# Kernel optimization log

Measured on AMD Instinct MI355X. Metric: run time of the kernel, lower is better.

## Reference

```python
import jax, jax.numpy as jnp
import numpy as np

COST_CLASS, COST_BBOX, COST_MASK = 1.0, 5.0, 2.0
EPS = 1e-6


def setup_inputs() -> dict:
    key = jax.random.key(0)
    k = jax.random.split(key, 8)
    B, Q, M, C1, H, W = 8, 300, 100, 81, 128, 128
    pred_logits = jax.random.normal(k[0], (B, Q, C1), jnp.float32)
    # boxes as valid xyxy in [0,1]: lo in [0,.5], size in [0,.5]
    plo = jax.random.uniform(k[1], (B, Q, 2)) * 0.5
    psz = jax.random.uniform(k[2], (B, Q, 2)) * 0.5
    pred_boxes = jnp.concatenate([plo, plo + psz], axis=-1)
    pred_masks = jax.random.normal(k[3], (B, Q, H, W), jnp.float32)
    gt_labels = jax.random.randint(k[4], (B, M), 0, C1, dtype=jnp.int32)
    glo = jax.random.uniform(k[5], (B, M, 2)) * 0.5
    gsz = jax.random.uniform(k[6], (B, M, 2)) * 0.5
    gt_boxes = jnp.concatenate([glo, glo + gsz], axis=-1)
    gt_masks = (jax.random.uniform(k[7], (B, M, H, W)) > 0.5).astype(jnp.float32)
    valid = jnp.ones((B, M), jnp.bool_)
    return dict(pred_logits=pred_logits, pred_boxes=pred_boxes, pred_masks=pred_masks,
                gt_labels=gt_labels, gt_boxes=gt_boxes, gt_masks=gt_masks, valid=valid)


def _giou(b1, b2):
    # b1 [Q,4], b2 [M,4] (xyxy) -> [Q,M] generalized IoU
    lt = jnp.maximum(b1[:, None, :2], b2[None, :, :2])
    rb = jnp.minimum(b1[:, None, 2:], b2[None, :, 2:])
    wh = jnp.clip(rb - lt, 0.0)
    inter = wh[..., 0] * wh[..., 1]
    a1 = (b1[:, 2] - b1[:, 0]) * (b1[:, 3] - b1[:, 1])
    a2 = (b2[:, 2] - b2[:, 0]) * (b2[:, 3] - b2[:, 1])
    union = a1[:, None] + a2[None, :] - inter
    iou = inter / (union + EPS)
    ltm = jnp.minimum(b1[:, None, :2], b2[None, :, :2])
    rbm = jnp.maximum(b1[:, None, 2:], b2[None, :, 2:])
    whm = jnp.clip(rbm - ltm, 0.0)
    am = whm[..., 0] * whm[..., 1]
    return iou - (am - union) / (am + EPS)


@jax.jit
def _cost_matrix(pred_logits, pred_boxes, pred_masks, gt_labels, gt_boxes, gt_masks):
    B, Q = pred_logits.shape[:2]
    M = gt_labels.shape[1]
    probs = jax.nn.softmax(pred_logits, axis=-1)                      # [B,Q,C+1]
    idx = jnp.broadcast_to(gt_labels[:, None, :].astype(jnp.int32), (B, Q, M))
    cost_class = -jnp.take_along_axis(probs, idx, axis=2)             # [B,Q,M]
    # L1 cdist
    cost_bbox = jnp.abs(pred_boxes[:, :, None, :] - gt_boxes[:, None, :, :]).sum(-1)
    cost_giou = -jax.vmap(_giou)(pred_boxes, gt_boxes)                # [B,Q,M]
    # dice cost
    pm = jax.nn.sigmoid(pred_masks).reshape(B, Q, -1)                 # [B,Q,HW]
    gm = gt_masks.reshape(B, M, -1).astype(pm.dtype)                  # [B,M,HW]
    num = 2.0 * jnp.einsum('bqc,bmc->bqm', pm, gm)
    den = pm.sum(-1)[:, :, None] + gm.sum(-1)[:, None, :]
    cost_mask = 1.0 - num / (den + EPS)
    # NOTE: faithful to source quirk -- giou term is folded into cost_bbox
    # and therefore weighted by COST_BBOX.
    return (COST_CLASS * cost_class + COST_BBOX * (cost_bbox + cost_giou)
            + COST_MASK * cost_mask)


def _hungarian(cost):
    # Jonker-Volgenant style shortest-augmenting-path assignment (e-maxx).
    # cost: np [n,m] with n <= m. Returns p[m]: row assigned to each col (-1 if none).
    n, m = cost.shape
    u = np.zeros(n)
    v = np.zeros(m)
    p = np.full(m, -1, np.int64)
    for i in range(n):
        minv = np.full(m, np.inf)
        way = np.full(m, -1, np.int64)
        used = np.zeros(m, bool)
        cur_row, j0 = i, -1
        while True:
            cur = cost[cur_row] - u[cur_row] - v
            upd = (~used) & (cur < minv)
            minv[upd] = cur[upd]
            way[upd] = j0
            mv = np.where(used, np.inf, minv)
            j1 = int(np.argmin(mv))
            delta = mv[j1]
            u[i] += delta
            uj = np.nonzero(used)[0]
            if uj.size:
                u[p[uj]] += delta
                v[uj] -= delta
            minv[~used] -= delta
            used[j1] = True
            j0 = j1
            cur_row = p[j1]
            if cur_row == -1:
                break
        j = j0
        while j != -1:
            jp = way[j]
            p[j] = p[jp] if jp != -1 else i
            j = jp
    return p


def reference(pred_logits, pred_boxes, pred_masks, gt_labels, gt_boxes, gt_masks, valid):
    # valid is all-ones (num_gt == max_objects for every sample), so the
    # per-sample variable-size slicing in the torch loop reduces to full M.
    C = _cost_matrix(pred_logits, pred_boxes, pred_masks, gt_labels, gt_boxes, gt_masks)
    Cn = np.asarray(C, dtype=np.float64)
    preds, gts = [], []
    for b in range(Cn.shape[0]):
        # solve on transpose: rows = gt (M=100) <= cols = queries (Q=300)
        p = _hungarian(Cn[b].T)            # p[q] = matched gt index or -1
        q = np.nonzero(p >= 0)[0]          # sorted pred indices (scipy convention)
        preds.append(q)
        gts.append(p[q])
    pred_idx = jnp.asarray(np.stack(preds), dtype=jnp.int32)  # [B, M]
    gt_idx = jnp.asarray(np.stack(gts), dtype=jnp.int32)      # [B, M]
    return C, pred_idx, gt_idx
```

## Files before the change

kernel.cpp:

```cpp
#include <hip/hip_runtime.h>

#define HW 16384
#define NQ 300
#define NM 100
#define NB 8
#define NC 81
#define KCH 1024
#define NKC 16
#define CTP 304

typedef __attribute__((ext_vector_type(8))) short frag8;
typedef __attribute__((ext_vector_type(4))) float float4v;
typedef __attribute__((ext_vector_type(4))) unsigned short ushort4v;

__device__ __forceinline__ unsigned short f2bf(float f) {
  union { float f; unsigned u; } c; c.f = f;
  unsigned r = c.u + 0x7FFFu + ((c.u >> 16) & 1u);
  return (unsigned short)(r >> 16);
}

__global__ __launch_bounds__(256) void prep_kernel(
    const float* __restrict__ pmask, const float* __restrict__ gmask,
    unsigned short* __restrict__ pm, unsigned short* __restrict__ gm,
    float* __restrict__ psum, float* __restrict__ gsum) {
  int row = blockIdx.x;
  int t = threadIdx.x;
  bool isP = row < NB * NQ;
  const float* srcf = isP ? (pmask + (size_t)row * HW)
                          : (gmask + (size_t)(row - NB * NQ) * HW);
  unsigned short* dst = isP ? (pm + (size_t)row * HW)
                            : (gm + (size_t)(row - NB * NQ) * HW);
  const float4v* src = (const float4v*)srcf;
  float s = 0.f;
  for (int i = t; i < HW / 4; i += 256) {
    float4v x = src[i];
    float y0, y1, y2, y3;
    if (isP) {
      y0 = 1.f / (1.f + __expf(-x.x));
      y1 = 1.f / (1.f + __expf(-x.y));
      y2 = 1.f / (1.f + __expf(-x.z));
      y3 = 1.f / (1.f + __expf(-x.w));
    } else { y0 = x.x; y1 = x.y; y2 = x.z; y3 = x.w; }
    s += (y0 + y1) + (y2 + y3);
    ushort4v o = { f2bf(y0), f2bf(y1), f2bf(y2), f2bf(y3) };
    *(ushort4v*)(dst + i * 4) = o;
  }
  for (int off = 32; off > 0; off >>= 1) s += __shfl_xor(s, off, 64);
  __shared__ float red[4];
  int wave = t >> 6, lane = t & 63;
  if (lane == 0) red[wave] = s;
  __syncthreads();
  if (t == 0) {
    float tot = (red[0] + red[1]) + (red[2] + red[3]);
    if (isP) psum[row] = tot; else gsum[row - NB * NQ] = tot;
  }
}

__global__ __launch_bounds__(256) void softmax_kernel(
    const float* __restrict__ logits, float* __restrict__ probs) {
  int wave = threadIdx.x >> 6, lane = threadIdx.x & 63;
  int row = blockIdx.x * 4 + wave;
  const float* in = logits + (size_t)row * NC;
  float x0 = (lane < NC) ? in[lane] : -1e30f;
  float x1 = (lane + 64 < NC) ? in[lane + 64] : -1e30f;
  float mx = fmaxf(x0, x1);
  for (int off = 32; off > 0; off >>= 1) mx = fmaxf(mx, __shfl_xor(mx, off, 64));
  float e0 = (lane < NC) ? __expf(x0 - mx) : 0.f;
  float e1 = (lane + 64 < NC) ? __expf(x1 - mx) : 0.f;
  float s = e0 + e1;
  for (int off = 32; off > 0; off >>= 1) s += __shfl_xor(s, off, 64);
  float inv = 1.f / s;
  if (lane < NC) probs[(size_t)row * NC + lane] = e0 * inv;
  if (lane + 64 < NC) probs[(size_t)row * NC + lane + 64] = e1 * inv;
}

__global__ __launch_bounds__(64) void dot_kernel(
    const unsigned short* __restrict__ pm, const unsigned short* __restrict__ gm,
    float* __restrict__ dotv) {
  int qt = blockIdx.x;
  int b = blockIdx.y >> 4, kc = blockIdx.y & 15;
  int lane = threadIdx.x;
  int q0 = qt * 16;
  int row_a = q0 + (lane & 15);
  int ra = (row_a < NQ) ? row_a : NQ - 1;
  int koff = (lane >> 4) * 8;
  const unsigned short* pA = pm + ((size_t)b * NQ + ra) * HW + kc * KCH + koff;
  const unsigned short* pB0 = gm + (size_t)b * NM * HW + kc * KCH + koff;
  const unsigned short* pB[7];
#pragma unroll
  for (int mt = 0; mt < 7; ++mt) {
    int row_b = mt * 16 + (lane & 15);
    int rb = (row_b < NM) ? row_b : NM - 1;
    pB[mt] = pB0 + (size_t)rb * HW;
  }
  float4v acc[7];
#pragma unroll
  for (int mt = 0; mt < 7; ++mt) acc[mt] = (float4v){0.f, 0.f, 0.f, 0.f};
#pragma unroll 2
  for (int k = 0; k < KCH; k += 32) {
    frag8 a = *(const frag8*)(pA + k);
#pragma unroll
    for (int mt = 0; mt < 7; ++mt) {
      frag8 bb = *(const frag8*)(pB[mt] + k);
      acc[mt] = __builtin_amdgcn_mfma_f32_16x16x32_bf16(a, bb, acc[mt], 0, 0, 0);
    }
  }
#pragma unroll
  for (int mt = 0; mt < 7; ++mt) {
    int cm = mt * 16 + (lane & 15);
    if (cm < NM) {
#pragma unroll
      for (int r = 0; r < 4; ++r) {
        int cq = q0 + (lane >> 4) * 4 + r;
        if (cq < NQ)
          unsafeAtomicAdd(&dotv[((size_t)b * NQ + cq) * NM + cm], acc[mt][r]);
      }
    }
  }
}

__global__ __launch_bounds__(256) void combine_kernel(
    const float* __restrict__ dotv, const float* __restrict__ psum,
    const float* __restrict__ gsum, const float* __restrict__ probs,
    const int* __restrict__ labels, const float* __restrict__ pboxes,
    const float* __restrict__ gboxes, float* __restrict__ outC,
    float* __restrict__ ct) {
  int idx = blockIdx.x * 256 + threadIdx.x;
  if (idx >= NB * NQ * NM) return;
  int b = idx / (NQ * NM);
  int r = idx - b * (NQ * NM);
  int q = r / NM;
  int m = r - q * NM;
  float num = 2.f * dotv[idx];
  float den = psum[b * NQ + q] + gsum[b * NM + m];
  float cmask = 1.f - num / (den + 1e-6f);
  int lab = labels[b * NM + m];
  float cclass = -probs[((size_t)b * NQ + q) * NC + lab];
  const float* pb = pboxes + ((size_t)b * NQ + q) * 4;
  const float* gb = gboxes + ((size_t)b * NM + m) * 4;
  float p0 = pb[0], p1 = pb[1], p2 = pb[2], p3 = pb[3];
  float g0 = gb[0], g1 = gb[1], g2 = gb[2], g3 = gb[3];
  float cbbox = fabsf(p0 - g0) + fabsf(p1 - g1) + fabsf(p2 - g2) + fabsf(p3 - g3);
  float iw = fmaxf(fminf(p2, g2) - fmaxf(p0, g0), 0.f);
  float ih = fmaxf(fminf(p3, g3) - fmaxf(p1, g1), 0.f);
  float inter = iw * ih;
  float a1 = (p2 - p0) * (p3 - p1), a2 = (g2 - g0) * (g3 - g1);
  float uni = a1 + a2 - inter;
  float iou = inter / (uni + 1e-6f);
  float aw = fmaxf(fmaxf(p2, g2) - fminf(p0, g0), 0.f);
  float ah = fmaxf(fmaxf(p3, g3) - fminf(p1, g1), 0.f);
  float am = aw * ah;
  float giou = iou - (am - uni) / (am + 1e-6f);
  float C = cclass + 5.f * (cbbox - giou) + 2.f * cmask;
  outC[idx] = C;
  ct[((size_t)b * NM + m) * CTP + q] = C;
}

extern __shared__ char hsmem[];
__global__ __launch_bounds__(64) void hungarian_kernel(
    const float* __restrict__ ct, float* __restrict__ out) {
  float* cost = (float*)hsmem;
  float* u = (float*)(hsmem + 121600);
  int* p = (int*)(hsmem + 122000);
  int* way = (int*)(hsmem + 123280);
  int* colA = (int*)(hsmem + 124560);
  int* rowUsed = (int*)(hsmem + 124960);
  int* colUsed = (int*)(hsmem + 125360);
  const int b = blockIdx.x;
  const int lane = threadIdx.x;
  const float* a = ct + (size_t)b * NM * CTP;

  for (int i = lane; i < NM * CTP; i += 64) cost[i] = a[i];
  for (int k = lane; k < NM; k += 64) rowUsed[k] = 0;
  float v[5], minv[5];
  int usedR[5];
#pragma unroll
  for (int w = 0; w < 5; ++w) {
    p[lane + 64 * w] = -1;
    colUsed[lane + 64 * w] = 0;
    v[w] = 0.f;
  }
  __syncthreads();

  for (int i = lane; i < NM; i += 64) {
    float mv = __builtin_inff();
    int cj = 0;
    for (int j = 0; j < NQ; ++j) {
      float c = cost[i * CTP + j];
      if (c < mv) { mv = c; cj = j; }
    }
    u[i] = mv;
    colA[i] = cj;
  }
  __syncthreads();
  if (lane == 0) {
    for (int i = 0; i < NM; ++i) {
      int j = colA[i];
      if (!colUsed[j]) { colUsed[j] = 1; p[j] = i; rowUsed[i] = 1; }
    }
  }
  __syncthreads();

  for (int i = 0; i < NM; ++i) {
    if (rowUsed[i]) continue;
#pragma unroll
    for (int w = 0; w < 5; ++w) {
      int j = lane + 64 * w;
      minv[w] = __builtin_inff();
      usedR[w] = (j >= NQ) ? 1 : 0;
      way[j] = -1;
    }
    int cur_row = i;
    int j0 = -1;
    __builtin_amdgcn_wave_barrier();
    while (true) {
      float urow = u[cur_row];
      unsigned long long best = ~0ull;
#pragma unroll
      for (int w = 0; w < 5; ++w) {
        if (!usedR[w]) {
          int j = lane + 64 * w;
          float cur = cost[cur_row * CTP + j] - urow - v[w];
          if (cur < minv[w]) { minv[w] = cur; way[j] = j0; }
          unsigned sb = __float_as_uint(minv[w]);
          sb = (sb >> 31) ? ~sb : (sb | 0x80000000u);
          unsigned long long key = ((unsigned long long)sb << 32) | (unsigned)j;
          if (key < best) best = key;
        }
      }
      for (int off = 32; off > 0; off >>= 1) {
        unsigned long long o = __shfl_xor(best, off, 64);
        if (o < best) best = o;
      }
      int j1 = (int)(best & 0xFFFFFFFFu);
      unsigned sb = (unsigned)(best >> 32);
      float delta = __uint_as_float((sb >> 31) ? (sb ^ 0x80000000u) : ~sb);
      __builtin_amdgcn_wave_barrier();
#pragma unroll
      for (int w = 0; w < 5; ++w) {
        int j = lane + 64 * w;
        if (j < NQ) {
          if (usedR[w]) {
            v[w] -= delta;
            int pj = p[j];
            u[pj] += delta;
          } else {
            minv[w] -= delta;
          }
        }
      }
      if (lane == 0) u[i] += delta;
      __builtin_amdgcn_wave_barrier();
#pragma unroll
      for (int w = 0; w < 5; ++w) {
        if (lane + 64 * w == j1) usedR[w] = 1;
      }
      int nr = p[j1];
      j0 = j1;
      if (nr < 0) break;
      cur_row = nr;
    }
    __builtin_amdgcn_wave_barrier();
    if (lane == 0) {
      int j = j0;
      while (j != -1) {
        int jp = way[j];
        p[j] = (jp != -1) ? p[jp] : i;
        j = jp;
      }
    }
    __syncthreads();
  }
  if (lane == 0) {
    float* po = out + NB * NQ * NM + b * NM;
    float* go = out + NB * NQ * NM + NB * NM + b * NM;
    int cnt = 0;
    for (int j = 0; j < NQ; ++j) {
      int pj = p[j];
      if (pj >= 0) { po[cnt] = (float)j; go[cnt] = (float)pj; ++cnt; }
    }
  }
}

extern "C" void kernel_launch(void* const* d_in, const int* in_sizes, int n_in,
                              void* d_out, int out_size, void* d_ws, size_t ws_size,
                              hipStream_t stream) {
  const float* logits = (const float*)d_in[0];
  const float* pboxes = (const float*)d_in[1];
  const float* pmask  = (const float*)d_in[2];
  const int*   labels = (const int*)d_in[3];
  const float* gboxes = (const float*)d_in[4];
  const float* gmask  = (const float*)d_in[5];
  float* out = (float*)d_out;
  char* ws = (char*)d_ws;

  unsigned short* pm   = (unsigned short*)(ws + 0);
  unsigned short* gmb  = (unsigned short*)(ws + 78643200);
  float* psum  = (float*)(ws + 104857600);
  float* gsum  = (float*)(ws + 104867200);
  float* probs = (float*)(ws + 104870400);
  float* dotv  = (float*)(ws + 105648000);
  float* ct    = (float*)(ws + 106608000);

  hipFuncSetAttribute(reinterpret_cast<const void*>(hungarian_kernel),
                      hipFuncAttributeMaxDynamicSharedMemorySize, 126640);

  hipMemsetAsync(dotv, 0, NB * NQ * NM * sizeof(float), stream);
  hipLaunchKernelGGL(prep_kernel, dim3(NB * NQ + NB * NM), dim3(256), 0, stream,
                     pmask, gmask, pm, gmb, psum, gsum);
  hipLaunchKernelGGL(softmax_kernel, dim3(600), dim3(256), 0, stream, logits, probs);
  hipLaunchKernelGGL(dot_kernel, dim3(19, NB * NKC), dim3(64), 0, stream, pm, gmb, dotv);
  hipLaunchKernelGGL(combine_kernel, dim3((NB * NQ * NM + 255) / 256), dim3(256), 0, stream,
                     dotv, psum, gsum, probs, labels, pboxes, gboxes, out, ct);
  hipLaunchKernelGGL(hungarian_kernel, dim3(NB), dim3(64), 126640, stream, ct, out);
}
```

Before: 519.6 us.

## Add auction-style augmenting-row reduction and lazy dual updates to Hungarian solver

Replaces the serial greedy column initialization with a parallel atomicMin-based assignment. It then adds a JVC-style augmenting row reduction pass that uses first/second minimum reductions over a queue of free rows, capped at 192 pops. The shortest-path phase now keeps cumulative distances and applies dual updates once at the end of each augmentation instead of on every step. The final index compaction is parallelized with ballots. The aim is to cut the serial single-wave Hungarian time, which likely dominates, at the cost of more complex logic. Tie-breaking may differ from the reference when there are equal-cost assignments.

```diff
diff --git a/kernel.cpp b/kernel.cpp
--- a/kernel.cpp
+++ b/kernel.cpp
@@ -159,70 +159,151 @@
 extern __shared__ char hsmem[];
 __global__ __launch_bounds__(64) void hungarian_kernel(
     const float* __restrict__ ct, float* __restrict__ out) {
-  float* cost = (float*)hsmem;
-  float* u = (float*)(hsmem + 121600);
-  int* p = (int*)(hsmem + 122000);
-  int* way = (int*)(hsmem + 123280);
-  int* colA = (int*)(hsmem + 124560);
-  int* rowUsed = (int*)(hsmem + 124960);
-  int* colUsed = (int*)(hsmem + 125360);
+  float* cost   = (float*)hsmem;
+  float* u      = (float*)(hsmem + 121600);
+  int*   p      = (int*)(hsmem + 122000);
+  int*   way    = (int*)(hsmem + 123280);
+  int*   colOwn = (int*)(hsmem + 124560);
+  int*   rowUsed= (int*)(hsmem + 125840);
+  int*   queue  = (int*)(hsmem + 126240);
+  int*   qmisc  = (int*)(hsmem + 127840);
   const int b = blockIdx.x;
   const int lane = threadIdx.x;
-  const float* a = ct + (size_t)b * NM * CTP;
-
-  for (int i = lane; i < NM * CTP; i += 64) cost[i] = a[i];
-  for (int k = lane; k < NM; k += 64) rowUsed[k] = 0;
-  float v[5], minv[5];
-  int usedR[5];
+  const float INF = __builtin_inff();
+
+  {
+    const float4v* a4 = (const float4v*)(ct + (size_t)b * NM * CTP);
+    float4v* c4 = (float4v*)cost;
+    for (int i = lane; i < NM * CTP / 4; i += 64) c4[i] = a4[i];
+  }
 #pragma unroll
   for (int w = 0; w < 5; ++w) {
     p[lane + 64 * w] = -1;
-    colUsed[lane + 64 * w] = 0;
-    v[w] = 0.f;
-  }
+    colOwn[lane + 64 * w] = 0x7fffffff;
+  }
+  if (lane == 0) { qmisc[0] = 0; qmisc[1] = 0; }
+  float v[5];
+#pragma unroll
+  for (int w = 0; w < 5; ++w) v[w] = 0.f;
   __syncthreads();
 
-  for (int i = lane; i < NM; i += 64) {
-    float mv = __builtin_inff();
-    int cj = 0;
+  int rarg0 = 0, rarg1 = 0;
+  {
+    int i = lane;
+    float mv = INF; int cj = 0;
     for (int j = 0; j < NQ; ++j) {
       float c = cost[i * CTP + j];
       if (c < mv) { mv = c; cj = j; }
     }
-    u[i] = mv;
-    colA[i] = cj;
-  }
+    u[i] = mv; rarg0 = cj;
+  }
+  if (lane < NM - 64) {
+    int i = lane + 64;
+    float mv = INF; int cj = 0;
+    for (int j = 0; j < NQ; ++j) {
+      float c = cost[i * CTP + j];
+      if (c < mv) { mv = c; cj = j; }
+    }
+    u[i] = mv; rarg1 = cj;
+  }
+  atomicMin(&colOwn[rarg0], lane);
+  if (lane < NM - 64) atomicMin(&colOwn[rarg1], lane + 64);
   __syncthreads();
-  if (lane == 0) {
-    for (int i = 0; i < NM; ++i) {
-      int j = colA[i];
-      if (!colUsed[j]) { colUsed[j] = 1; p[j] = i; rowUsed[i] = 1; }
+  int free0 = 0, free1 = 0;
+  {
+    bool won = (colOwn[rarg0] == lane);
+    if (won) p[rarg0] = lane;
+    rowUsed[lane] = won ? 1 : 0;
+    free0 = won ? 0 : 1;
+  }
+  if (lane < NM - 64) {
+    bool won = (colOwn[rarg1] == lane + 64);
+    if (won) p[rarg1] = lane + 64;
+    rowUsed[lane + 64] = won ? 1 : 0;
+    free1 = won ? 0 : 1;
+  }
+  {
+    unsigned long long m0 = __ballot(free0 != 0);
+    if (free0) queue[__popcll(m0 & ((1ull << lane) - 1ull))] = lane;
+    int base = (int)__popcll(m0);
+    unsigned long long m1 = __ballot(free1 != 0);
+    if (free1) queue[base + (int)__popcll(m1 & ((1ull << lane) - 1ull))] = lane + 64;
+    base += (int)__popcll(m1);
+    if (lane == 0) qmisc[1] = base;
+  }
+
+  int pops = 0;
+  while (true) {
+    __syncthreads();
+    int h = qmisc[0], t = qmisc[1];
+    if (h >= t || pops >= 192) break;
+    int i = queue[h];
+    ++pops;
+    if (lane == 0) qmisc[0] = h + 1;
+    float m1 = INF, m2 = INF; int jl = 0;
+#pragma unroll
+    for (int w = 0; w < 5; ++w) {
+      int j = lane + 64 * w;
+      float tt = (j < NQ) ? (cost[i * CTP + j] - v[w]) : INF;
+      if (tt < m1) { m2 = m1; m1 = tt; jl = j; } else if (tt < m2) m2 = tt;
+    }
+    unsigned long long best;
+    {
+      unsigned sb = __float_as_uint(m1);
+      sb = (sb >> 31) ? ~sb : (sb | 0x80000000u);
+      best = ((unsigned long long)sb << 32) | (unsigned)jl;
+    }
+    for (int off = 32; off > 0; off >>= 1) {
+      unsigned long long o = __shfl_xor(best, off, 64);
+      if (o < best) best = o;
+    }
+    int j1 = (int)(best & 0xFFFFFFFFu);
+    float m1g;
+    {
+      unsigned sb = (unsigned)(best >> 32);
+      m1g = __uint_as_float((sb >> 31) ? (sb ^ 0x80000000u) : ~sb);
+    }
+    float c2 = (jl == j1) ? m2 : m1;
+    for (int off = 32; off > 0; off >>= 1) c2 = fminf(c2, __shfl_xor(c2, off, 64));
+    float delta = (c2 > m1g) ? (c2 - m1g) : 0.f;
+    int i1 = p[j1];
+    if (i1 >= 0 && delta <= 0.f) {
+      if (lane == 0) u[i] = c2;
+      continue;
+    }
+#pragma unroll
+    for (int w = 0; w < 5; ++w) if (lane + 64 * w == j1) v[w] -= delta;
+    if (lane == 0) {
+      u[i] = c2;
+      p[j1] = i;
+      rowUsed[i] = 1;
+      if (i1 >= 0) { rowUsed[i1] = 0; queue[t] = i1; qmisc[1] = t + 1; }
     }
   }
   __syncthreads();
 
   for (int i = 0; i < NM; ++i) {
     if (rowUsed[i]) continue;
+    float dv[5]; int usedR[5];
 #pragma unroll
     for (int w = 0; w < 5; ++w) {
       int j = lane + 64 * w;
-      minv[w] = __builtin_inff();
+      dv[w] = INF;
       usedR[w] = (j >= NQ) ? 1 : 0;
       way[j] = -1;
     }
-    int cur_row = i;
-    int j0 = -1;
-    __builtin_amdgcn_wave_barrier();
+    float S = 0.f;
+    int nr = i, j0 = -1;
     while (true) {
-      float urow = u[cur_row];
+      float urow = u[nr];
       unsigned long long best = ~0ull;
 #pragma unroll
       for (int w = 0; w < 5; ++w) {
         if (!usedR[w]) {
           int j = lane + 64 * w;
-          float cur = cost[cur_row * CTP + j] - urow - v[w];
-          if (cur < minv[w]) { minv[w] = cur; way[j] = j0; }
-          unsigned sb = __float_as_uint(minv[w]);
+          float cand = S + cost[nr * CTP + j] - urow - v[w];
+          if (cand < dv[w]) { dv[w] = cand; way[j] = j0; }
+          unsigned sb = __float_as_uint(dv[w]);
           sb = (sb >> 31) ? ~sb : (sb | 0x80000000u);
           unsigned long long key = ((unsigned long long)sb << 32) | (unsigned)j;
           if (key < best) best = key;
@@ -233,34 +314,29 @@
         if (o < best) best = o;
       }
       int j1 = (int)(best & 0xFFFFFFFFu);
-      unsigned sb = (unsigned)(best >> 32);
-      float delta = __uint_as_float((sb >> 31) ? (sb ^ 0x80000000u) : ~sb);
-      __builtin_amdgcn_wave_barrier();
-#pragma unroll
-      for (int w = 0; w < 5; ++w) {
-        int j = lane + 64 * w;
-        if (j < NQ) {
-          if (usedR[w]) {
-            v[w] -= delta;
-            int pj = p[j];
-            u[pj] += delta;
-          } else {
-            minv[w] -= delta;
-          }
-        }
-      }
-      if (lane == 0) u[i] += delta;
-      __builtin_amdgcn_wave_barrier();
-#pragma unroll
-      for (int w = 0; w < 5; ++w) {
-        if (lane + 64 * w == j1) usedR[w] = 1;
-      }
-      int nr = p[j1];
+      {
+        unsigned sb = (unsigned)(best >> 32);
+        S = __uint_as_float((sb >> 31) ? (sb ^ 0x80000000u) : ~sb);
+      }
+#pragma unroll
+      for (int w = 0; w < 5; ++w) if (lane + 64 * w == j1) usedR[w] = 1;
       j0 = j1;
-      if (nr < 0) break;
-      cur_row = nr;
-    }
-    __builtin_amdgcn_wave_barrier();
+      int nr2 = p[j1];
+      if (nr2 < 0) break;
+      nr = nr2;
+    }
+#pragma unroll
+    for (int w = 0; w < 5; ++w) {
+      int j = lane + 64 * w;
+      if (j < NQ && usedR[w]) {
+        float amt = S - dv[w];
+        v[w] -= amt;
+        int pj = p[j];
+        if (pj >= 0) u[pj] += amt;
+      }
+    }
+    if (lane == 0) u[i] += S;
+    __syncthreads();
     if (lane == 0) {
       int j = j0;
       while (j != -1) {
@@ -268,16 +344,26 @@
         p[j] = (jp != -1) ? p[jp] : i;
         j = jp;
       }
+      rowUsed[i] = 1;
     }
     __syncthreads();
   }
-  if (lane == 0) {
+
+  {
     float* po = out + NB * NQ * NM + b * NM;
     float* go = out + NB * NQ * NM + NB * NM + b * NM;
-    int cnt = 0;
-    for (int j = 0; j < NQ; ++j) {
-      int pj = p[j];
-      if (pj >= 0) { po[cnt] = (float)j; go[cnt] = (float)pj; ++cnt; }
+    int base = 0;
+#pragma unroll
+    for (int w = 0; w < 5; ++w) {
+      int j = lane + 64 * w;
+      int pj = (j < NQ) ? p[j] : -1;
+      unsigned long long mask = __ballot(pj >= 0);
+      if (pj >= 0) {
+        int pos = base + (int)__popcll(mask & ((1ull << lane) - 1ull));
+        po[pos] = (float)j;
+        go[pos] = (float)pj;
+      }
+      base += (int)__popcll(mask);
     }
   }
 }
@@ -303,7 +389,7 @@
   float* ct    = (float*)(ws + 106608000);
 
   hipFuncSetAttribute(reinterpret_cast<const void*>(hungarian_kernel),
-                      hipFuncAttributeMaxDynamicSharedMemorySize, 126640);
+                      hipFuncAttributeMaxDynamicSharedMemorySize, 127872);
 
   hipMemsetAsync(dotv, 0, NB * NQ * NM * sizeof(float), stream);
   hipLaunchKernelGGL(prep_kernel, dim3(NB * NQ + NB * NM), dim3(256), 0, stream,
@@ -312,5 +398,5 @@
   hipLaunchKernelGGL(dot_kernel, dim3(19, NB * NKC), dim3(64), 0, stream, pm, gmb, dotv);
   hipLaunchKernelGGL(combine_kernel, dim3((NB * NQ * NM + 255) / 256), dim3(256), 0, stream,
                      dotv, psum, gsum, probs, labels, pboxes, gboxes, out, ct);
-  hipLaunchKernelGGL(hungarian_kernel, dim3(NB), dim3(64), 126640, stream, ct, out);
-}
+  hipLaunchKernelGGL(hungarian_kernel, dim3(NB), dim3(64), 127872, stream, ct, out);
+}
```

After: 524.6 us. About the same (+1.0%).
